# Kernel optimization log

Hardware: AMD Instinct MI355X
Metric: run time of the kernel (lower is better)

Reference implementation:

```python
import jax, jax.numpy as jnp
import numpy as np

T = 0.5  # temperature from __init__


def setup_inputs() -> dict:
    key = jax.random.key(0)
    k1, k2, k3 = jax.random.split(key, 3)
    n, d = 8192, 256
    findings_embeddings = jax.random.normal(k1, (n, d), dtype=jnp.float32)
    impression_embeddings = jax.random.normal(k2, (n, d), dtype=jnp.float32)
    chexpert_label = jax.random.randint(k3, (n,), 0, 14, dtype=jnp.int64)
    return {
        "findings_embeddings": findings_embeddings,
        "impression_embeddings": impression_embeddings,
        "chexpert_label": chexpert_label,
    }


def reference(findings_embeddings, impression_embeddings, chexpert_label):
    n = findings_embeddings.shape[0]
    # [n, n] similarity matrix scaled by temperature
    logits = jnp.matmul(findings_embeddings, impression_embeddings.T) / T
    # zero out entries where labels match, except the diagonal (i != j)
    eq = chexpert_label[:, None] == chexpert_label[None, :]
    off_diag_eq = eq & ~jnp.eye(n, dtype=bool)
    logits = jnp.where(off_diag_eq, 0.0, logits)
    # trace(log_softmax_row + log_softmax_col) without materializing two [n,n] copies:
    # diag(log_softmax(L, axis)) = diag(L) - logsumexp(L, axis)
    diag = jnp.diagonal(logits)
    lse_row = jax.nn.logsumexp(logits, axis=1)  # findings -> impression direction
    lse_col = jax.nn.logsumexp(logits, axis=0)  # impression -> findings direction
    loss = -jnp.sum((diag - lse_row) + (diag - lse_col)) / n
    return loss
```

## Files before the change

### kernel.cpp

```cpp
#include <hip/hip_runtime.h>
#include <hip/hip_bf16.h>

#define N 8192
#define D 256
#define NSLICE 32
#define BM 256
#define TROWS 4
#define COLS_PER_SLICE (N / NSLICE)
#define NSTRIP (COLS_PER_SLICE / 16)
#define NRB (N / BM)

#define CSHIFT 160.0f
#define K2LOG2E 2.885390082f
#define LN2F 0.6931471805599453f

typedef __attribute__((ext_vector_type(4))) float f32x4;

__device__ inline float fast_exp2(float x) { return __builtin_amdgcn_exp2f(x); }
__device__ inline float fast_log2(float x) { return __builtin_amdgcn_logf(x); }

__device__ inline unsigned int pack_fp8x4(float a, float b, float c, float d) {
    unsigned int p = __builtin_amdgcn_cvt_pk_fp8_f32(a, b, 0, 0);
    p = __builtin_amdgcn_cvt_pk_fp8_f32(c, d, (int)p, 1);
    return p;
}

__global__ void convert_fp8(const float* __restrict__ F, const float* __restrict__ Imp,
                            unsigned int* __restrict__ Fb8, unsigned int* __restrict__ Ib8) {
    const int i = blockIdx.x * blockDim.x + threadIdx.x;
    const float* src = (blockIdx.y == 0) ? F : Imp;
    unsigned int* dst = (blockIdx.y == 0) ? Fb8 : Ib8;
    const int l = i & 63;
    const int ks = (i >> 6) & 7;
    const int g = i >> 9;
    const int row = g * 16 + (l & 15);
    const int k0 = ks * 32 + (l >> 4) * 8;
    const float* p = src + (size_t)row * D + k0;
    const float4 v0 = *reinterpret_cast<const float4*>(p);
    const float4 v1 = *reinterpret_cast<const float4*>(p + 4);
    dst[i * 2] = pack_fp8x4(v0.x, v0.y, v0.z, v0.w);
    dst[i * 2 + 1] = pack_fp8x4(v1.x, v1.y, v1.z, v1.w);
}

__launch_bounds__(256, 2)
__global__ void tile_pass(const unsigned char* __restrict__ Fb8,
                          const unsigned char* __restrict__ Ib8,
                          const int* __restrict__ labels,
                          float* __restrict__ partials_row,
                          float* __restrict__ partials_col) {
    __shared__ float colacc[4][COLS_PER_SLICE];
    __shared__ int labs[COLS_PER_SLICE];

    const int tid = threadIdx.x;
    const int lane = tid & 63;
    const int wave = tid >> 6;
    const int rb = blockIdx.x;
    const int row0 = rb * BM + wave * (16 * TROWS);
    const int rg0 = row0 >> 4;
    const int c0 = blockIdx.y * COLS_PER_SLICE;
    const int cg0 = c0 >> 4;
    const int lrow = lane & 15;
    const int kgrp = lane >> 4;

    for (int i = tid; i < COLS_PER_SLICE; i += 256) {
        labs[i] = labels[c0 + i];
        colacc[0][i] = 0.f; colacc[1][i] = 0.f; colacc[2][i] = 0.f; colacc[3][i] = 0.f;
    }

    long afrag[TROWS][8];
#pragma unroll
    for (int t = 0; t < TROWS; ++t)
#pragma unroll
        for (int ks = 0; ks < 8; ++ks)
            afrag[t][ks] = *reinterpret_cast<const long*>(
                Fb8 + (size_t)(rg0 + t) * 4096 + ks * 512 + lane * 8);

    int labr[TROWS][4];
#pragma unroll
    for (int t = 0; t < TROWS; ++t) {
        const int base = row0 + t * 16 + kgrp * 4;
#pragma unroll
        for (int r = 0; r < 4; ++r) labr[t][r] = labels[base + r];
    }

    float s[TROWS][4];
#pragma unroll
    for (int t = 0; t < TROWS; ++t)
#pragma unroll
        for (int r = 0; r < 4; ++r) s[t][r] = 0.0f;

    __syncthreads();

#define LOADB(buf, st)                                                          \
    {                                                                           \
        const unsigned char* sb = Ib8 + (size_t)(cg0 + (st)) * 4096 + lane * 8; \
        _Pragma("unroll")                                                       \
        for (int ks = 0; ks < 8; ++ks)                                          \
            buf[ks] = *reinterpret_cast<const long*>(sb + ks * 512);            \
    }

#define MFMA_STRIP(acc, buf)                                                    \
    {                                                                           \
        _Pragma("unroll")                                                       \
        for (int t = 0; t < TROWS; ++t) acc[t] = f32x4{0.f, 0.f, 0.f, 0.f};     \
        _Pragma("unroll")                                                       \
        for (int ks = 0; ks < 8; ++ks)                                          \
            _Pragma("unroll")                                                   \
            for (int t = 0; t < TROWS; ++t)                                     \
                acc[t] = __builtin_amdgcn_mfma_f32_16x16x32_fp8_fp8(            \
                    afrag[t][ks], buf[ks], acc[t], 0, 0, 0);                    \
    }

#define EPI(acc, st)                                                            \
    {                                                                           \
        const int labc = labs[(st) * 16 + lrow];                                \
        float colpart = 0.0f;                                                   \
        _Pragma("unroll")                                                       \
        for (int t = 0; t < TROWS; ++t) {                                       \
            _Pragma("unroll")                                                   \
            for (int r = 0; r < 4; ++r) {                                       \
                float arg = __builtin_fmaf(acc[t][r], K2LOG2E, -CSHIFT);        \
                arg = (labr[t][r] == labc) ? -1000.0f : arg;                    \
                float e = fast_exp2(arg);                                       \
                s[t][r] += e;                                                   \
                colpart += e;                                                   \
            }                                                                   \
        }                                                                       \
        colpart += __shfl_xor(colpart, 16, 64);                                 \
        colpart += __shfl_xor(colpart, 32, 64);                                 \
        if (kgrp == 0) colacc[wave][(st) * 16 + lrow] += colpart;               \
    }

    long b0[8], b1[8];
    f32x4 acc0[TROWS], acc1[TROWS];

    LOADB(b0, 0);
    LOADB(b1, 1);
    MFMA_STRIP(acc0, b0);

#pragma unroll 1
    for (int st = 0; st < NSTRIP; st += 2) {
        if (st + 2 < NSTRIP) LOADB(b0, st + 2);
        MFMA_STRIP(acc1, b1);
        EPI(acc0, st);
        if (st + 3 < NSTRIP) LOADB(b1, st + 3);
        if (st + 2 < NSTRIP) MFMA_STRIP(acc0, b0);
        EPI(acc1, st + 1);
    }
#undef LOADB
#undef MFMA_STRIP
#undef EPI

#pragma unroll
    for (int off = 1; off < 16; off <<= 1) {
#pragma unroll
        for (int t = 0; t < TROWS; ++t)
#pragma unroll
            for (int r = 0; r < 4; ++r)
                s[t][r] += __shfl_xor(s[t][r], off, 64);
    }
    if (lrow == 0) {
#pragma unroll
        for (int t = 0; t < TROWS; ++t)
#pragma unroll
            for (int r = 0; r < 4; ++r) {
                const int grow = row0 + t * 16 + kgrp * 4 + r;
                partials_row[(size_t)grow * NSLICE + blockIdx.y] = s[t][r];
            }
    }

    __syncthreads();
    for (int i = tid; i < COLS_PER_SLICE; i += 256) {
        float v = colacc[0][i] + colacc[1][i] + colacc[2][i] + colacc[3][i];
        partials_col[(size_t)rb * N + c0 + i] = v;
    }
}

__global__ void col_reduce(const float* __restrict__ partials_col, float* __restrict__ colsum,
                           const int* __restrict__ labels, int* __restrict__ counts) {
    if (blockIdx.x == NRB) {
        const int lane = threadIdx.x & 63;
        const int wave = threadIdx.x >> 6;
        int c = 0;
        for (int i = wave * 2048 + lane; i < wave * 2048 + 2048; i += 64) {
            const int lab = labels[i];
#pragma unroll
            for (int b = 0; b < 14; ++b) {
                unsigned long long m = __ballot(lab == b);
                if (lane == b) c += __popcll(m);
            }
        }
        __shared__ int wc[4][16];
        if (lane < 16) wc[wave][lane] = (lane < 14) ? c : 0;
        __syncthreads();
        if (threadIdx.x < 16)
            counts[threadIdx.x] = wc[0][threadIdx.x] + wc[1][threadIdx.x] +
                                  wc[2][threadIdx.x] + wc[3][threadIdx.x];
        return;
    }
    const int c = blockIdx.x * 256 + threadIdx.x;
    float v = 0.0f;
    for (int rbi = 0; rbi < NRB; ++rbi) v += partials_col[(size_t)rbi * N + c];
    colsum[c] = v;
}

__device__ inline float final_lse(float S, float cntlog, float diag) {
    float l1 = (S > 0.0f) ? (CSHIFT + fast_log2(S)) * LN2F : -INFINITY;
    float M = fmaxf(fmaxf(l1, cntlog), diag);
    return M + __logf(__expf(l1 - M) + __expf(cntlog - M) + __expf(diag - M));
}

__global__ void row_contrib(const float* __restrict__ F, const float* __restrict__ Imp,
                            const float* __restrict__ partials_row,
                            const float* __restrict__ colsum,
                            const int* __restrict__ counts,
                            const int* __restrict__ labels, float* __restrict__ blockSums) {
    const int lane = threadIdx.x & 63;
    const int wave = threadIdx.x >> 6;
    const int row = blockIdx.x * 4 + wave;

    float4 a = reinterpret_cast<const float4*>(F + (size_t)row * D)[lane];
    float4 b = reinterpret_cast<const float4*>(Imp + (size_t)row * D)[lane];
    float dot = a.x * b.x + a.y * b.y + a.z * b.z + a.w * b.w;
#pragma unroll
    for (int off = 32; off > 0; off >>= 1) dot += __shfl_xor(dot, off, 64);

    float sr = (lane < NSLICE) ? partials_row[(size_t)row * NSLICE + lane] : 0.0f;
#pragma unroll
    for (int off = 16; off > 0; off >>= 1) sr += __shfl_xor(sr, off, 64);

    __shared__ float sums[4];
    if (lane == 0) {
        const float diag = 2.0f * dot;
        const int cnt = counts[labels[row]] - 1;
        const float cntlog = (cnt > 0) ? __logf((float)cnt) : -INFINITY;
        const float S_col = colsum[row];
        const float lse_total = final_lse(sr, cntlog, diag) + final_lse(S_col, cntlog, diag);
        sums[wave] = 2.0f * diag - lse_total;
    }
    __syncthreads();
    if (threadIdx.x == 0)
        blockSums[blockIdx.x] = sums[0] + sums[1] + sums[2] + sums[3];
}

__global__ void final_reduce(const float* __restrict__ blockSums, float* __restrict__ out) {
    __shared__ float red[256];
    float v = 0.0f;
    for (int i = threadIdx.x; i < N / 4; i += 256) v += blockSums[i];
    red[threadIdx.x] = v;
    __syncthreads();
    for (int st = 128; st > 0; st >>= 1) {
        if (threadIdx.x < st) red[threadIdx.x] += red[threadIdx.x + st];
        __syncthreads();
    }
    if (threadIdx.x == 0) out[0] = -red[0] / (float)N;
}

extern "C" void kernel_launch(void* const* d_in, const int* in_sizes, int n_in,
                              void* d_out, int out_size, void* d_ws, size_t ws_size,
                              hipStream_t stream) {
    const float* F = (const float*)d_in[0];
    const float* Imp = (const float*)d_in[1];
    const int* labels = (const int*)d_in[2];
    float* out = (float*)d_out;

    char* ws = (char*)d_ws;
    size_t off = 0;
    unsigned char* Fb8 = (unsigned char*)(ws + off); off += (size_t)N * D;
    unsigned char* Ib8 = (unsigned char*)(ws + off); off += (size_t)N * D;
    float* partials_row = (float*)(ws + off); off += (size_t)N * NSLICE * 4;
    float* partials_col = (float*)(ws + off); off += (size_t)NRB * N * 4;
    float* colsum = (float*)(ws + off); off += (size_t)N * 4;
    float* blockSums = (float*)(ws + off); off += (size_t)(N / 4) * 4;
    int* counts = (int*)(ws + off);

    dim3 cgrid(N * D / 8 / 256, 2);
    convert_fp8<<<cgrid, 256, 0, stream>>>(F, Imp, (unsigned int*)Fb8, (unsigned int*)Ib8);

    dim3 g(NRB, NSLICE);
    tile_pass<<<g, 256, 0, stream>>>(Fb8, Ib8, labels, partials_row, partials_col);

    col_reduce<<<NRB + 1, 256, 0, stream>>>(partials_col, colsum, labels, counts);
    row_contrib<<<N / 4, 256, 0, stream>>>(F, Imp, partials_row, colsum, counts, labels, blockSums);
    final_reduce<<<1, 256, 0, stream>>>(blockSums, out);
}
```

Baseline: 61.74 us.

## Fuse column reduction via atomics, precompute diagonal and counts in convert kernel

Removes the col_reduce kernel by having tile_pass atomically add per-block column sums into a zeroed colsum buffer, and moves label counting, colsum zeroing and the diagonal dot products into extra blocks of the fp8 convert kernel. row_contrib now reads a precomputed diagonal instead of re-reading both fp32 embedding matrices. NSLICE is halved, so each block covers twice as many columns with a larger shared-memory footprint and half as many blocks. The exchange is one fewer launch and less partial-buffer traffic, against atomic contention and nondeterministic summation order.

```diff
diff --git a/kernel.cpp b/kernel.cpp
--- a/kernel.cpp
+++ b/kernel.cpp
@@ -3,7 +3,7 @@
 
 #define N 8192
 #define D 256
-#define NSLICE 32
+#define NSLICE 16
 #define BM 256
 #define TROWS 4
 #define COLS_PER_SLICE (N / NSLICE)
@@ -26,20 +26,59 @@
 }
 
 __global__ void convert_fp8(const float* __restrict__ F, const float* __restrict__ Imp,
-                            unsigned int* __restrict__ Fb8, unsigned int* __restrict__ Ib8) {
-    const int i = blockIdx.x * blockDim.x + threadIdx.x;
-    const float* src = (blockIdx.y == 0) ? F : Imp;
-    unsigned int* dst = (blockIdx.y == 0) ? Fb8 : Ib8;
-    const int l = i & 63;
-    const int ks = (i >> 6) & 7;
-    const int g = i >> 9;
-    const int row = g * 16 + (l & 15);
-    const int k0 = ks * 32 + (l >> 4) * 8;
-    const float* p = src + (size_t)row * D + k0;
-    const float4 v0 = *reinterpret_cast<const float4*>(p);
-    const float4 v1 = *reinterpret_cast<const float4*>(p + 4);
-    dst[i * 2] = pack_fp8x4(v0.x, v0.y, v0.z, v0.w);
-    dst[i * 2 + 1] = pack_fp8x4(v1.x, v1.y, v1.z, v1.w);
+                            unsigned int* __restrict__ Fb8, unsigned int* __restrict__ Ib8,
+                            const int* __restrict__ labels, int* __restrict__ counts,
+                            float* __restrict__ diagArr, float* __restrict__ colsum) {
+    const int tid = threadIdx.x;
+    if (blockIdx.y < 2) {
+        const int i = blockIdx.x * blockDim.x + tid;
+        const float* src = (blockIdx.y == 0) ? F : Imp;
+        unsigned int* dst = (blockIdx.y == 0) ? Fb8 : Ib8;
+        const int l = i & 63;
+        const int ks = (i >> 6) & 7;
+        const int g = i >> 9;
+        const int row = g * 16 + (l & 15);
+        const int k0 = ks * 32 + (l >> 4) * 8;
+        const float* p = src + (size_t)row * D + k0;
+        const float4 v0 = *reinterpret_cast<const float4*>(p);
+        const float4 v1 = *reinterpret_cast<const float4*>(p + 4);
+        dst[i * 2] = pack_fp8x4(v0.x, v0.y, v0.z, v0.w);
+        dst[i * 2 + 1] = pack_fp8x4(v1.x, v1.y, v1.z, v1.w);
+        return;
+    }
+    const int row = blockIdx.x * 8 + (tid >> 5);
+    const int sl = tid & 31;
+    const float* fr = F + (size_t)row * D + sl * 8;
+    const float* ir = Imp + (size_t)row * D + sl * 8;
+    const float4 f0 = *reinterpret_cast<const float4*>(fr);
+    const float4 f1 = *reinterpret_cast<const float4*>(fr + 4);
+    const float4 i0 = *reinterpret_cast<const float4*>(ir);
+    const float4 i1 = *reinterpret_cast<const float4*>(ir + 4);
+    float dot = f0.x * i0.x + f0.y * i0.y + f0.z * i0.z + f0.w * i0.w +
+                f1.x * i1.x + f1.y * i1.y + f1.z * i1.z + f1.w * i1.w;
+#pragma unroll
+    for (int off = 16; off > 0; off >>= 1) dot += __shfl_xor(dot, off, 64);
+    if (sl == 0) diagArr[row] = dot;
+    if (tid < 8) colsum[blockIdx.x * 8 + tid] = 0.0f;
+
+    if (blockIdx.x == 0) {
+        const int lane = tid & 63;
+        const int wave = tid >> 6;
+        int c = 0;
+        for (int i = wave * 2048 + lane; i < wave * 2048 + 2048; i += 64) {
+            const int lab = labels[i];
+#pragma unroll
+            for (int b = 0; b < 14; ++b) {
+                unsigned long long m = __ballot(lab == b);
+                if (lane == b) c += __popcll(m);
+            }
+        }
+        __shared__ int wc[4][16];
+        if (lane < 16) wc[wave][lane] = (lane < 14) ? c : 0;
+        __syncthreads();
+        if (tid < 16)
+            counts[tid] = wc[0][tid] + wc[1][tid] + wc[2][tid] + wc[3][tid];
+    }
 }
 
 __launch_bounds__(256, 2)
@@ -47,7 +86,7 @@
                           const unsigned char* __restrict__ Ib8,
                           const int* __restrict__ labels,
                           float* __restrict__ partials_row,
-                          float* __restrict__ partials_col) {
+                          float* __restrict__ colsum) {
     __shared__ float colacc[4][COLS_PER_SLICE];
     __shared__ int labs[COLS_PER_SLICE];
 
@@ -172,36 +211,8 @@
     __syncthreads();
     for (int i = tid; i < COLS_PER_SLICE; i += 256) {
         float v = colacc[0][i] + colacc[1][i] + colacc[2][i] + colacc[3][i];
-        partials_col[(size_t)rb * N + c0 + i] = v;
-    }
-}
-
-__global__ void col_reduce(const float* __restrict__ partials_col, float* __restrict__ colsum,
-                           const int* __restrict__ labels, int* __restrict__ counts) {
-    if (blockIdx.x == NRB) {
-        const int lane = threadIdx.x & 63;
-        const int wave = threadIdx.x >> 6;
-        int c = 0;
-        for (int i = wave * 2048 + lane; i < wave * 2048 + 2048; i += 64) {
-            const int lab = labels[i];
-#pragma unroll
-            for (int b = 0; b < 14; ++b) {
-                unsigned long long m = __ballot(lab == b);
-                if (lane == b) c += __popcll(m);
-            }
-        }
-        __shared__ int wc[4][16];
-        if (lane < 16) wc[wave][lane] = (lane < 14) ? c : 0;
-        __syncthreads();
-        if (threadIdx.x < 16)
-            counts[threadIdx.x] = wc[0][threadIdx.x] + wc[1][threadIdx.x] +
-                                  wc[2][threadIdx.x] + wc[3][threadIdx.x];
-        return;
-    }
-    const int c = blockIdx.x * 256 + threadIdx.x;
-    float v = 0.0f;
-    for (int rbi = 0; rbi < NRB; ++rbi) v += partials_col[(size_t)rbi * N + c];
-    colsum[c] = v;
+        atomicAdd(&colsum[c0 + i], v);
+    }
 }
 
 __device__ inline float final_lse(float S, float cntlog, float diag) {
@@ -210,7 +221,7 @@
     return M + __logf(__expf(l1 - M) + __expf(cntlog - M) + __expf(diag - M));
 }
 
-__global__ void row_contrib(const float* __restrict__ F, const float* __restrict__ Imp,
+__global__ void row_contrib(const float* __restrict__ diagArr,
                             const float* __restrict__ partials_row,
                             const float* __restrict__ colsum,
                             const int* __restrict__ counts,
@@ -219,19 +230,13 @@
     const int wave = threadIdx.x >> 6;
     const int row = blockIdx.x * 4 + wave;
 
-    float4 a = reinterpret_cast<const float4*>(F + (size_t)row * D)[lane];
-    float4 b = reinterpret_cast<const float4*>(Imp + (size_t)row * D)[lane];
-    float dot = a.x * b.x + a.y * b.y + a.z * b.z + a.w * b.w;
-#pragma unroll
-    for (int off = 32; off > 0; off >>= 1) dot += __shfl_xor(dot, off, 64);
-
     float sr = (lane < NSLICE) ? partials_row[(size_t)row * NSLICE + lane] : 0.0f;
 #pragma unroll
     for (int off = 16; off > 0; off >>= 1) sr += __shfl_xor(sr, off, 64);
 
     __shared__ float sums[4];
     if (lane == 0) {
-        const float diag = 2.0f * dot;
+        const float diag = 2.0f * diagArr[row];
         const int cnt = counts[labels[row]] - 1;
         const float cntlog = (cnt > 0) ? __logf((float)cnt) : -INFINITY;
         const float S_col = colsum[row];
@@ -269,18 +274,18 @@
     unsigned char* Fb8 = (unsigned char*)(ws + off); off += (size_t)N * D;
     unsigned char* Ib8 = (unsigned char*)(ws + off); off += (size_t)N * D;
     float* partials_row = (float*)(ws + off); off += (size_t)N * NSLICE * 4;
-    float* partials_col = (float*)(ws + off); off += (size_t)NRB * N * 4;
     float* colsum = (float*)(ws + off); off += (size_t)N * 4;
+    float* diagArr = (float*)(ws + off); off += (size_t)N * 4;
     float* blockSums = (float*)(ws + off); off += (size_t)(N / 4) * 4;
     int* counts = (int*)(ws + off);
 
-    dim3 cgrid(N * D / 8 / 256, 2);
-    convert_fp8<<<cgrid, 256, 0, stream>>>(F, Imp, (unsigned int*)Fb8, (unsigned int*)Ib8);
+    dim3 cgrid(N * D / 8 / 256, 3);
+    convert_fp8<<<cgrid, 256, 0, stream>>>(F, Imp, (unsigned int*)Fb8, (unsigned int*)Ib8,
+                                           labels, counts, diagArr, colsum);
 
     dim3 g(NRB, NSLICE);
-    tile_pass<<<g, 256, 0, stream>>>(Fb8, Ib8, labels, partials_row, partials_col);
-
-    col_reduce<<<NRB + 1, 256, 0, stream>>>(partials_col, colsum, labels, counts);
-    row_contrib<<<N / 4, 256, 0, stream>>>(F, Imp, partials_row, colsum, counts, labels, blockSums);
+    tile_pass<<<g, 256, 0, stream>>>(Fb8, Ib8, labels, partials_row, colsum);
+
+    row_contrib<<<N / 4, 256, 0, stream>>>(diagArr, partials_row, colsum, counts, labels, blockSums);
     final_reduce<<<1, 256, 0, stream>>>(blockSums, out);
 }
```

Measured after the change: 57.26 us (median of 2 runs). -7.3%, faster.
